# Kernel tuning notes

Hardware: AMD Instinct MI355X
Metric: run time of the kernel (lower is better)

## Reference

```python
import jax, jax.numpy as jnp
import numpy as np
import math

NZ, NX, NY = 4, 2048, 2048
DX = DY = 4000.0


def dstI1D(x):
    # type-I discrete sine transform along last axis (ortho norm) via irfft
    n = x.shape[-1]
    pad = [(0, 0)] * (x.ndim - 1) + [(1, 1)]
    return jnp.fft.irfft(-1j * jnp.pad(x, pad), axis=-1, norm='ortho')[..., 1:n + 1]


def dstI2D(x):
    # DST-I over the last two axes
    x = dstI1D(x)
    x = jnp.swapaxes(dstI1D(jnp.swapaxes(x, -1, -2)), -1, -2)
    return x


def inverse_elliptic_dstI(f, helmholtz_dst):
    # DST-I is its own inverse with ortho norm: solve in spectral space
    return dstI2D(dstI2D(f) / helmholtz_dst)


def center_avg_2D(x):
    return 0.25 * (x[..., 1:, 1:] + x[..., 1:, :-1] + x[..., :-1, 1:] + x[..., :-1, :-1])


def _build_solver_constants(beta):
    # create_helmholtz_dst
    x, y = jnp.meshgrid(jnp.arange(1, NY), jnp.arange(1, NX), indexing='ij')
    L_mat = (2 * (jnp.cos(math.pi / NX * x) - 1) / DX ** 2
             + 2 * (jnp.cos(math.pi / NY * y) - 1) / DY ** 2)
    H_mat = (L_mat[None] - beta[:, None, None]).astype(jnp.float32)  # [Nz, Nx-1, Ny-1]
    # compute_homogeneous_solution
    ones_int = jnp.ones((NZ, NX - 1, NY - 1), jnp.float32)
    sol = inverse_elliptic_dstI(ones_int, H_mat)
    sol = jnp.pad(sol, ((0, 0), (1, 1), (1, 1)))  # [Nz, Nx+1, Ny+1]
    homsol = jnp.ones((NZ, NX + 1, NY + 1), jnp.float32) + sol * beta[:, None, None]
    homsol_mean = jnp.mean(center_avg_2D(homsol), axis=(-2, -1))  # mask = all ones
    return H_mat, homsol.astype(jnp.float32), homsol_mean.astype(jnp.float32)


def setup_inputs() -> dict:
    key = jax.random.key(0)
    k1, k2 = jax.random.split(key)
    q = jax.random.normal(k1, (NZ, NX - 1, NY - 1), jnp.float32)
    # mode<->layer change of basis (Mode2LayerTransformer): Cm2l = inv(Cl2m)
    A = jax.random.normal(k2, (NZ, NZ), jnp.float32) * 0.3 + jnp.eye(NZ, dtype=jnp.float32)
    Cl2m = A
    Cm2l = jnp.linalg.inv(A).astype(jnp.float32)
    # lambda_sq eigenvalues (1/deformation-radius^2), first barotropic mode ~ 0
    beta = jnp.array([0.0, 1.0e-9, 4.0e-9, 1.0e-8], jnp.float32)
    H_mat, homsol, homsol_mean = _build_solver_constants(beta)
    return {'q': q, 'Cl2m': Cl2m, 'Cm2l': Cm2l,
            'helmholtz_mat': H_mat, 'homsol': homsol, 'homsol_mean': homsol_mean}


def reference(q, Cl2m, Cm2l, helmholtz_mat, homsol, homsol_mean):
    # layer -> mode
    src_modes = jnp.einsum('ml,lxy->mxy', Cl2m, q)
    # spectral elliptic solve per mode (Nz batched over leading axis)
    psi_modes = inverse_elliptic_dstI(src_modes, helmholtz_mat)
    psi_modes = jnp.pad(psi_modes, ((0, 0), (1, 1), (1, 1)))  # [Nz, Nx+1, Ny+1]
    # homogeneous-solution correction to enforce zero mean
    psi_modes_mean = jnp.mean(center_avg_2D(psi_modes), axis=(-2, -1))
    alpha = -psi_modes_mean / homsol_mean
    psi_modes = psi_modes + alpha[:, None, None] * homsol
    # mode -> layer
    psi = jnp.einsum('lm,mxy->lxy', Cm2l, psi_modes)
    return psi
```

## Files before the change

### kernel.cpp

```cpp
#include <hip/hip_runtime.h>


typedef __attribute__((ext_vector_type(8))) short bf16x8;
typedef __attribute__((ext_vector_type(4))) float f32x4;
typedef __attribute__((ext_vector_type(8))) unsigned short ushort8;
typedef __attribute__((ext_vector_type(4))) unsigned short ushort4v;
typedef __attribute__((ext_vector_type(2))) float float2v;

#define LDS_SPACE __attribute__((address_space(3)))
#define GLB_SPACE __attribute__((address_space(1)))

__device__ __forceinline__ void gld_lds16(const unsigned short* g, unsigned short* l) {
  __builtin_amdgcn_global_load_lds((const GLB_SPACE void*)g, (LDS_SPACE void*)l, 16, 0, 0);
}

__device__ __forceinline__ float sinrev(float rev) {
  float r;
  asm("v_sin_f32 %0, %1" : "=v"(r) : "v"(rev));
  return r;
}

__device__ __forceinline__ unsigned short f2b(float f) {
  union { float f; unsigned u; } v; v.f = f;
  unsigned r = (v.u + 0x7fffu + ((v.u >> 16) & 1u)) >> 16;
  return (unsigned short)r;
}
__device__ __forceinline__ float b2f(unsigned short u) {
  union { unsigned u; float f; } v; v.u = ((unsigned)u) << 16;
  return v.f;
}

__global__ __launch_bounds__(256)
void tables_kernel(unsigned short* __restrict__ T) {
  const int base = (blockIdx.x * 256 + threadIdx.x) * 4;
  const int tbl = base >> 20, n = (base >> 10) & 1023, k0 = base & 1023;
  const int cp1 = (tbl & 1) ? 2 * n + 2 : 2 * n + 1;
  ushort4v v;
#pragma unroll
  for (int e = 0; e < 4; ++e) {
    const int k = k0 + e;
    int a;
    if (tbl < 2) a = k;
    else a = (k < 512) ? 2 * k : (k < 1023 ? 2 * (k - 512) + 1 : 1023);
    const int ph = ((a + 1) * cp1) & 4095;
    v[e] = f2b(0.03125f * sinrev((float)ph * (1.0f / 4096.0f)));
  }
  *(ushort4v*)&T[base] = v;
}

__global__ __launch_bounds__(256)
void mix_fold(const float* __restrict__ q, const float* __restrict__ Cl2m,
              unsigned short* __restrict__ AE, unsigned short* __restrict__ AO) {
  const int idx = blockIdx.x * 256 + threadIdx.x;
  const int x = idx >> 10, u = idx & 1023;
  float c[16];
#pragma unroll
  for (int i = 0; i < 16; ++i) c[i] = Cl2m[i];
  float fe[4] = {0.f, 0.f, 0.f, 0.f}, fo[4] = {0.f, 0.f, 0.f, 0.f};
  if (x < 2047) {
#pragma unroll
    for (int l = 0; l < 4; ++l) {
      const size_t base = ((size_t)l * 2047 + x) * 2047;
      const float qa = q[base + u];
      const float qb = (u < 1023) ? q[base + 2046 - u] : 0.f;
      const float E = (u == 1023) ? qa : qa + qb;
      const float O = (u == 1023) ? 0.f : qa - qb;
#pragma unroll
      for (int m = 0; m < 4; ++m) { fe[m] += c[m * 4 + l] * E; fo[m] += c[m * 4 + l] * O; }
    }
  }
#pragma unroll
  for (int m = 0; m < 4; ++m) {
    AE[((size_t)m * 2048 + x) * 1024 + u] = f2b(fe[m]);
    AO[((size_t)m * 2048 + x) * 1024 + u] = f2b(fo[m]);
  }
}

template <int MAP>
__global__ __launch_bounds__(256)
void tfold(const unsigned short* __restrict__ in, unsigned short* __restrict__ outE,
           unsigned short* __restrict__ outO) {
  __shared__ unsigned short t1[64][72];
  __shared__ unsigned short t2[64][72];
  const size_t ib = (size_t)blockIdx.z * (2048u * 2048u);
  const size_t ob = (size_t)blockIdx.z * (2048u * 1024u);
  const int c0 = blockIdx.x * 64, u0 = blockIdx.y * 64;
  const int t = threadIdx.x;
  const int rr = t >> 3, cc = (t & 7) * 8;
#pragma unroll
  for (int ch = 0; ch < 2; ++ch) {
    const int r = ch * 32 + rr, u = u0 + r;
    const int r1 = (MAP == 0) ? u : (u < 512 ? u : 1024 + (u - 512));
    const int r2 = (MAP == 0) ? 2046 - u : (u < 512 ? 1023 - u : 2046 - (u - 512));
    ushort8 v1 = *(const ushort8*)&in[ib + (size_t)r1 * 2048 + c0 + cc];
    ushort8 v2 = *(const ushort8*)&in[ib + (size_t)r2 * 2048 + c0 + cc];
#pragma unroll
    for (int j = 0; j < 8; ++j) { t1[r][cc + j] = v1[j]; t2[r][cc + j] = v2[j]; }
  }
  __syncthreads();
#pragma unroll
  for (int ch = 0; ch < 2; ++ch) {
    const int r = ch * 32 + rr;
    ushort8 vE, vO;
#pragma unroll
    for (int j = 0; j < 8; ++j) {
      const int uu = u0 + cc + j;
      const float a = b2f(t1[cc + j][r]);
      const float b = b2f(t2[cc + j][r]);
      vE[j] = f2b((uu == 1023) ? a : a + b);
      vO[j] = f2b((uu == 1023) ? 0.f : a - b);
    }
    const size_t o = ob + (size_t)(c0 + r) * 1024 + u0 + cc;
    *(ushort8*)&outE[o] = vE;
    *(ushort8*)&outO[o] = vO;
  }
}

__global__ __launch_bounds__(256)
void fold_cols(const unsigned short* __restrict__ R, unsigned short* __restrict__ AE,
               unsigned short* __restrict__ AO) {
  const int idx = blockIdx.x * 256 + threadIdx.x;
  const int row = idx >> 10, u = idx & 1023;
  const int c1 = (u < 512) ? u : (u < 1023 ? 512 + u : 1535);
  const int c2 = (u < 512) ? 1023 - u : (u < 1023 ? 2558 - u : 1535);
  const float a = b2f(R[(size_t)row * 2048 + c1]);
  const float b = b2f(R[(size_t)row * 2048 + c2]);
  AE[(size_t)row * 1024 + u] = f2b((u == 1023) ? a : a + b);
  AO[(size_t)row * 1024 + u] = f2b((u == 1023) ? 0.f : a - b);
}

#define MFMA_BF16 __builtin_amdgcn_mfma_f32_16x16x32_bf16

template <int EPI>
__global__ __launch_bounds__(512, 2)
void gemm_eo(const unsigned short* __restrict__ A, const unsigned short* __restrict__ T,
             unsigned short* __restrict__ Cb, const float* __restrict__ H,
             float* __restrict__ sums) {
  __shared__ __align__(16) char lds[131072];
  const int bid = blockIdx.x;
  const int swz = (bid & 7) * 32 + (bid >> 3);
  const int h = swz & 1;
  const int bn = (swz >> 1) & 3, bm = swz >> 3;
  const int tid = threadIdx.x;
  const int lane = tid & 63, wave = tid >> 6;
  const int wr = wave >> 2, wc = wave & 3;
  const int lr = lane & 15, kg = lane >> 4;
  const int x7 = lr & 7;

  const unsigned short* gA = A + (size_t)h * 8388608u + (size_t)bm * 256 * 1024;
  const unsigned short* gB = T + (size_t)h * 1048576u + (size_t)bn * 256 * 1024;

  const int row0 = tid >> 3;
  const int slot = (tid & 7) ^ (row0 & 7);

  auto stage = [&](int kt, int c) {
    char* lc = lds + c * 65536;
    const size_t ko = (size_t)kt * 64 + slot * 8;
#pragma unroll
    for (int i = 0; i < 4; ++i)
      gld_lds16(gA + (size_t)(row0 + i * 64) * 1024 + ko,
                (unsigned short*)(lc + (tid + i * 512) * 16));
#pragma unroll
    for (int i = 0; i < 4; ++i)
      gld_lds16(gB + (size_t)(row0 + i * 64) * 1024 + ko,
                (unsigned short*)(lc + 32768 + (tid + i * 512) * 16));
  };

  f32x4 acc[8][4];
#pragma unroll
  for (int m = 0; m < 8; ++m)
#pragma unroll
    for (int n = 0; n < 4; ++n) acc[m][n] = (f32x4){0.f, 0.f, 0.f, 0.f};

  stage(0, 0);
  stage(1, 1);
  __syncthreads();

  const int arow = wr * 128 + lr;
  const int brow = wc * 64 + lr;
  const LDS_SPACE char* lbase = (const LDS_SPACE char*)lds;

  for (int t = 0; t < 16; ++t) {
    const LDS_SPACE char* la = lbase + (t & 1) * 65536;
    const LDS_SPACE char* lb = la + 32768;

    bf16x8 al[4][2], ah[4][2], bl[2][2], bh[2][2];

#pragma unroll
    for (int m = 0; m < 4; ++m)
#pragma unroll
      for (int ks = 0; ks < 2; ++ks)
        al[m][ks] = *(const LDS_SPACE bf16x8*)(la + (arow + m * 16) * 128 + (((ks * 4 + kg) ^ x7) << 4));
#pragma unroll
    for (int n = 0; n < 2; ++n)
#pragma unroll
      for (int ks = 0; ks < 2; ++ks)
        bl[n][ks] = *(const LDS_SPACE bf16x8*)(lb + (brow + n * 16) * 128 + (((ks * 4 + kg) ^ x7) << 4));
#pragma unroll
    for (int ks = 0; ks < 2; ++ks)
#pragma unroll
      for (int m = 0; m < 4; ++m)
#pragma unroll
        for (int n = 0; n < 2; ++n)
          acc[m][n] = MFMA_BF16(al[m][ks], bl[n][ks], acc[m][n], 0, 0, 0);

#pragma unroll
    for (int n = 0; n < 2; ++n)
#pragma unroll
      for (int ks = 0; ks < 2; ++ks)
        bh[n][ks] = *(const LDS_SPACE bf16x8*)(lb + (brow + (n + 2) * 16) * 128 + (((ks * 4 + kg) ^ x7) << 4));
#pragma unroll
    for (int ks = 0; ks < 2; ++ks)
#pragma unroll
      for (int m = 0; m < 4; ++m)
#pragma unroll
        for (int n = 0; n < 2; ++n)
          acc[m][n + 2] = MFMA_BF16(al[m][ks], bh[n][ks], acc[m][n + 2], 0, 0, 0);

#pragma unroll
    for (int m = 0; m < 4; ++m)
#pragma unroll
      for (int ks = 0; ks < 2; ++ks)
        ah[m][ks] = *(const LDS_SPACE bf16x8*)(la + (arow + (m + 4) * 16) * 128 + (((ks * 4 + kg) ^ x7) << 4));
#pragma unroll
    for (int ks = 0; ks < 2; ++ks)
#pragma unroll
      for (int m = 0; m < 4; ++m)
#pragma unroll
        for (int n = 0; n < 2; ++n)
          acc[m + 4][n + 2] = MFMA_BF16(ah[m][ks], bh[n][ks], acc[m + 4][n + 2], 0, 0, 0);
#pragma unroll
    for (int ks = 0; ks < 2; ++ks)
#pragma unroll
      for (int m = 0; m < 4; ++m)
#pragma unroll
        for (int n = 0; n < 2; ++n)
          acc[m + 4][n] = MFMA_BF16(ah[m][ks], bl[n][ks], acc[m + 4][n], 0, 0, 0);

    __syncthreads();
    if (t < 14) stage(t + 2, t & 1);
  }

  float beta = 0.f, tA[4];
  bool iok[4] = {true, true, true, true};
  if (EPI == 1) {
    const float s1 = sinrev(1.0f / 8192.0f);
    beta = -5.0e-7f * s1 * s1 - H[(size_t)(bm >> 3) * 4190209u];
#pragma unroll
    for (int n = 0; n < 4; ++n) {
      const int ia = 2 * (bn * 256 + wc * 64 + n * 16 + lr) + h;
      iok[n] = ia < 2047;
      const float s = sinrev((float)(ia + 1) * (1.0f / 8192.0f));
      tA[n] = -2.5e-7f * s * s;
    }
  }

  float ssum = 0.f;
#pragma unroll
  for (int m = 0; m < 8; ++m) {
#pragma unroll
    for (int j = 0; j < 4; ++j) {
      const int row_l = wr * 128 + m * 16 + kg * 4 + j;
      float tB = 0.f;
      bool jok = true;
      if (EPI == 1) {
        const int jint = (bm * 256 + row_l) & 2047;
        const int j_true = 2 * (jint & 1023) + (jint >> 10);
        jok = j_true < 2047;
        const float s = sinrev((float)(j_true + 1) * (1.0f / 8192.0f));
        tB = -2.5e-7f * s * s;
      }
#pragma unroll
      for (int n = 0; n < 4; ++n) {
        const int col_l = wc * 64 + n * 16 + lr;
        float v = acc[m][n][j];
        if (EPI == 1) {
          const float Hv = tA[n] + tB - beta;
          float r = __builtin_amdgcn_rcpf(Hv);
          r = r * (2.0f - Hv * r);
          v = (iok[n] && jok) ? v * r : 0.f;
        }
        if (EPI == 2) ssum += v;
        const int byte = row_l * 512 + ((((col_l >> 3) ^ (row_l & 7)) << 4)) + (col_l & 7) * 2;
        *(unsigned short*)&lds[byte] = f2b(v);
      }
    }
  }
  __syncthreads();

  unsigned short* gC = Cb + (size_t)(bm * 256) * 2048 + h * 1024 + bn * 256;
#pragma unroll
  for (int p = 0; p < 16; ++p) {
    const int c = p * 512 + tid;
    const int r = c >> 5, c16 = c & 31;
    const bf16x8 vv = *(const bf16x8*)&lds[r * 512 + ((c16 ^ (r & 7)) << 4)];
    *(bf16x8*)&gC[(size_t)r * 2048 + c16 * 8] = vv;
  }

  if (EPI == 2) {
#pragma unroll
    for (int off = 32; off > 0; off >>= 1) ssum += __shfl_xor(ssum, off);
    if (lane == 0) atomicAdd(&sums[bm >> 3], ssum);
  }
}

__global__ __launch_bounds__(256)
void final_kernel(const unsigned short* __restrict__ V, const float* __restrict__ homsol,
                  const float* __restrict__ hm, const float* __restrict__ Cm2l,
                  const float* __restrict__ sums, float* __restrict__ out) {
  const int pp = blockIdx.x * 256 + threadIdx.x;
  if (pp >= 2049 * 1025) return;
  const int x = pp / 1025, yy = pp - x * 1025;
  const int y0 = 2 * yy;
  const bool has1 = (y0 + 1) <= 2048;
  const bool xin = (x >= 1) && (x <= 2047);
  const bool in0 = xin && (yy >= 1) && (y0 <= 2047);
  const bool in1 = xin && has1 && (y0 + 1 <= 2047);
  const int row = (x >= 1) ? (((x - 1) & 1) ? 1024 + ((x - 1) >> 1) : ((x - 1) >> 1)) : 0;
  const int col0 = 1024 + yy - 1;
  const int col1 = yy;
  const size_t p0 = (size_t)x * 2049 + y0;

  float pm0[4], pm1[4];
#pragma unroll
  for (int m = 0; m < 4; ++m) {
    const size_t vb = (size_t)m * 4194304u + (size_t)row * 2048;
    const float i0 = in0 ? b2f(V[vb + col0]) : 0.f;
    const float i1 = in1 ? b2f(V[vb + col1]) : 0.f;
    const float alpha = -(sums[m] * (1.0f / 4194304.0f)) / hm[m];
    const size_t hb = (size_t)m * 4198401u + p0;
    pm0[m] = i0 + alpha * homsol[hb];
    pm1[m] = has1 ? (i1 + alpha * homsol[hb + 1]) : 0.f;
  }
#pragma unroll
  for (int l = 0; l < 4; ++l) {
    const float o0 = Cm2l[l * 4 + 0] * pm0[0] + Cm2l[l * 4 + 1] * pm0[1] +
                     Cm2l[l * 4 + 2] * pm0[2] + Cm2l[l * 4 + 3] * pm0[3];
    const size_t ob = (size_t)l * 4198401u + p0;
    if (has1) {
      const float o1 = Cm2l[l * 4 + 0] * pm1[0] + Cm2l[l * 4 + 1] * pm1[1] +
                       Cm2l[l * 4 + 2] * pm1[2] + Cm2l[l * 4 + 3] * pm1[3];
      float2v o; o[0] = o0; o[1] = o1;
      *(float2v*)&out[ob] = o;
    } else {
      out[ob] = o0;
    }
  }
}

extern "C" void kernel_launch(void* const* d_in, const int* in_sizes, int n_in,
                              void* d_out, int out_size, void* d_ws, size_t ws_size,
                              hipStream_t stream) {
  const float* q     = (const float*)d_in[0];
  const float* Cl2m  = (const float*)d_in[1];
  const float* Cm2l  = (const float*)d_in[2];
  const float* H     = (const float*)d_in[3];
  const float* hom   = (const float*)d_in[4];
  const float* hmean = (const float*)d_in[5];
  float* out = (float*)d_out;

  char* ws = (char*)d_ws;
  unsigned short* Tb = (unsigned short*)ws;
  unsigned short* Aslot = (unsigned short*)(ws + 8388608u);
  unsigned short* Bslot = (unsigned short*)(ws + 41943040u);
  float* sums        = (float*)(ws + 75497472u);
  unsigned short* AO = Aslot + 8388608u;

  tables_kernel<<<4096, 256, 0, stream>>>(Tb);
  mix_fold<<<8192, 256, 0, stream>>>(q, Cl2m, Aslot, AO);
  hipMemsetAsync(sums, 0, 16, stream);

  const dim3 tg(32, 16, 4);
  gemm_eo<0><<<256, 512, 0, stream>>>(Aslot, Tb, Bslot, nullptr, nullptr);
  tfold<0><<<tg, 256, 0, stream>>>(Bslot, Aslot, AO);
  gemm_eo<1><<<256, 512, 0, stream>>>(Aslot, Tb, Bslot, H, nullptr);
  fold_cols<<<32768, 256, 0, stream>>>(Bslot, Aslot, AO);
  gemm_eo<0><<<256, 512, 0, stream>>>(Aslot, Tb + 2097152u, Bslot, nullptr, nullptr);
  tfold<1><<<tg, 256, 0, stream>>>(Bslot, Aslot, AO);
  gemm_eo<2><<<256, 512, 0, stream>>>(Aslot, Tb + 2097152u, Bslot, nullptr, sums);

  final_kernel<<<8205, 256, 0, stream>>>(Bslot, hom, hmean, Cm2l, sums, out);
}
```

Baseline: 265.1 us.

## Split GEMM block tile across sixteen waves with smaller per-wave tiles

The even/odd DST GEMM kernels now launch 1024-thread blocks (16 waves) instead of 512. Each wave computes a 64x64 sub-tile rather than 128x64, which halves the accumulator registers per thread. Staging and output write-back loops are re-indexed for the larger block. The aim is more waves in flight to hide LDS and MFMA latency. In exchange, the operand reuse from each LDS fragment load per wave drops. The launch_bounds(1024,4) hint may also push the compiler to a tight register cap and risk spills.

```diff
diff --git a/kernel.cpp b/kernel.cpp
--- a/kernel.cpp
+++ b/kernel.cpp
@@ -132,7 +132,7 @@
 #define MFMA_BF16 __builtin_amdgcn_mfma_f32_16x16x32_bf16
 
 template <int EPI>
-__global__ __launch_bounds__(512, 2)
+__global__ __launch_bounds__(1024, 4)
 void gemm_eo(const unsigned short* __restrict__ A, const unsigned short* __restrict__ T,
              unsigned short* __restrict__ Cb, const float* __restrict__ H,
              float* __restrict__ sums) {
@@ -157,18 +157,18 @@
     char* lc = lds + c * 65536;
     const size_t ko = (size_t)kt * 64 + slot * 8;
 #pragma unroll
-    for (int i = 0; i < 4; ++i)
-      gld_lds16(gA + (size_t)(row0 + i * 64) * 1024 + ko,
-                (unsigned short*)(lc + (tid + i * 512) * 16));
-#pragma unroll
-    for (int i = 0; i < 4; ++i)
-      gld_lds16(gB + (size_t)(row0 + i * 64) * 1024 + ko,
-                (unsigned short*)(lc + 32768 + (tid + i * 512) * 16));
+    for (int i = 0; i < 2; ++i)
+      gld_lds16(gA + (size_t)(row0 + i * 128) * 1024 + ko,
+                (unsigned short*)(lc + (tid + i * 1024) * 16));
+#pragma unroll
+    for (int i = 0; i < 2; ++i)
+      gld_lds16(gB + (size_t)(row0 + i * 128) * 1024 + ko,
+                (unsigned short*)(lc + 32768 + (tid + i * 1024) * 16));
   };
 
-  f32x4 acc[8][4];
-#pragma unroll
-  for (int m = 0; m < 8; ++m)
+  f32x4 acc[4][4];
+#pragma unroll
+  for (int m = 0; m < 4; ++m)
 #pragma unroll
     for (int n = 0; n < 4; ++n) acc[m][n] = (f32x4){0.f, 0.f, 0.f, 0.f};
 
@@ -176,7 +176,7 @@
   stage(1, 1);
   __syncthreads();
 
-  const int arow = wr * 128 + lr;
+  const int arow = wr * 64 + lr;
   const int brow = wc * 64 + lr;
   const LDS_SPACE char* lbase = (const LDS_SPACE char*)lds;
 
@@ -184,58 +184,21 @@
     const LDS_SPACE char* la = lbase + (t & 1) * 65536;
     const LDS_SPACE char* lb = la + 32768;
 
-    bf16x8 al[4][2], ah[4][2], bl[2][2], bh[2][2];
-
-#pragma unroll
-    for (int m = 0; m < 4; ++m)
-#pragma unroll
-      for (int ks = 0; ks < 2; ++ks)
-        al[m][ks] = *(const LDS_SPACE bf16x8*)(la + (arow + m * 16) * 128 + (((ks * 4 + kg) ^ x7) << 4));
-#pragma unroll
-    for (int n = 0; n < 2; ++n)
-#pragma unroll
-      for (int ks = 0; ks < 2; ++ks)
-        bl[n][ks] = *(const LDS_SPACE bf16x8*)(lb + (brow + n * 16) * 128 + (((ks * 4 + kg) ^ x7) << 4));
-#pragma unroll
-    for (int ks = 0; ks < 2; ++ks)
+#pragma unroll
+    for (int ks = 0; ks < 2; ++ks) {
+      bf16x8 av[4], bv[4];
 #pragma unroll
       for (int m = 0; m < 4; ++m)
-#pragma unroll
-        for (int n = 0; n < 2; ++n)
-          acc[m][n] = MFMA_BF16(al[m][ks], bl[n][ks], acc[m][n], 0, 0, 0);
-
-#pragma unroll
-    for (int n = 0; n < 2; ++n)
-#pragma unroll
-      for (int ks = 0; ks < 2; ++ks)
-        bh[n][ks] = *(const LDS_SPACE bf16x8*)(lb + (brow + (n + 2) * 16) * 128 + (((ks * 4 + kg) ^ x7) << 4));
-#pragma unroll
-    for (int ks = 0; ks < 2; ++ks)
+        av[m] = *(const LDS_SPACE bf16x8*)(la + (arow + m * 16) * 128 + (((ks * 4 + kg) ^ x7) << 4));
+#pragma unroll
+      for (int n = 0; n < 4; ++n)
+        bv[n] = *(const LDS_SPACE bf16x8*)(lb + (brow + n * 16) * 128 + (((ks * 4 + kg) ^ x7) << 4));
 #pragma unroll
       for (int m = 0; m < 4; ++m)
 #pragma unroll
-        for (int n = 0; n < 2; ++n)
-          acc[m][n + 2] = MFMA_BF16(al[m][ks], bh[n][ks], acc[m][n + 2], 0, 0, 0);
-
-#pragma unroll
-    for (int m = 0; m < 4; ++m)
-#pragma unroll
-      for (int ks = 0; ks < 2; ++ks)
-        ah[m][ks] = *(const LDS_SPACE bf16x8*)(la + (arow + (m + 4) * 16) * 128 + (((ks * 4 + kg) ^ x7) << 4));
-#pragma unroll
-    for (int ks = 0; ks < 2; ++ks)
-#pragma unroll
-      for (int m = 0; m < 4; ++m)
-#pragma unroll
-        for (int n = 0; n < 2; ++n)
-          acc[m + 4][n + 2] = MFMA_BF16(ah[m][ks], bh[n][ks], acc[m + 4][n + 2], 0, 0, 0);
-#pragma unroll
-    for (int ks = 0; ks < 2; ++ks)
-#pragma unroll
-      for (int m = 0; m < 4; ++m)
-#pragma unroll
-        for (int n = 0; n < 2; ++n)
-          acc[m + 4][n] = MFMA_BF16(ah[m][ks], bl[n][ks], acc[m + 4][n], 0, 0, 0);
+        for (int n = 0; n < 4; ++n)
+          acc[m][n] = MFMA_BF16(av[m], bv[n], acc[m][n], 0, 0, 0);
+    }
 
     __syncthreads();
     if (t < 14) stage(t + 2, t & 1);
@@ -257,10 +220,10 @@
 
   float ssum = 0.f;
 #pragma unroll
-  for (int m = 0; m < 8; ++m) {
+  for (int m = 0; m < 4; ++m) {
 #pragma unroll
     for (int j = 0; j < 4; ++j) {
-      const int row_l = wr * 128 + m * 16 + kg * 4 + j;
+      const int row_l = wr * 64 + m * 16 + kg * 4 + j;
       float tB = 0.f;
       bool jok = true;
       if (EPI == 1) {
@@ -290,8 +253,8 @@
 
   unsigned short* gC = Cb + (size_t)(bm * 256) * 2048 + h * 1024 + bn * 256;
 #pragma unroll
-  for (int p = 0; p < 16; ++p) {
-    const int c = p * 512 + tid;
+  for (int p = 0; p < 8; ++p) {
+    const int c = p * 1024 + tid;
     const int r = c >> 5, c16 = c & 31;
     const bf16x8 vv = *(const bf16x8*)&lds[r * 512 + ((c16 ^ (r & 7)) << 4)];
     *(bf16x8*)&gC[(size_t)r * 2048 + c16 * 8] = vv;
@@ -371,13 +334,13 @@
   hipMemsetAsync(sums, 0, 16, stream);
 
   const dim3 tg(32, 16, 4);
-  gemm_eo<0><<<256, 512, 0, stream>>>(Aslot, Tb, Bslot, nullptr, nullptr);
+  gemm_eo<0><<<256, 1024, 0, stream>>>(Aslot, Tb, Bslot, nullptr, nullptr);
   tfold<0><<<tg, 256, 0, stream>>>(Bslot, Aslot, AO);
-  gemm_eo<1><<<256, 512, 0, stream>>>(Aslot, Tb, Bslot, H, nullptr);
+  gemm_eo<1><<<256, 1024, 0, stream>>>(Aslot, Tb, Bslot, H, nullptr);
   fold_cols<<<32768, 256, 0, stream>>>(Bslot, Aslot, AO);
-  gemm_eo<0><<<256, 512, 0, stream>>>(Aslot, Tb + 2097152u, Bslot, nullptr, nullptr);
+  gemm_eo<0><<<256, 1024, 0, stream>>>(Aslot, Tb + 2097152u, Bslot, nullptr, nullptr);
   tfold<1><<<tg, 256, 0, stream>>>(Bslot, Aslot, AO);
-  gemm_eo<2><<<256, 512, 0, stream>>>(Aslot, Tb + 2097152u, Bslot, nullptr, sums);
+  gemm_eo<2><<<256, 1024, 0, stream>>>(Aslot, Tb + 2097152u, Bslot, nullptr, sums);
 
   final_kernel<<<8205, 256, 0, stream>>>(Bslot, hom, hmean, Cm2l, sums, out);
 }
```

Result: slower. 301.4 us (+13.7%).
